# Performance work log

Measured on AMD Instinct MI355X. Metric: run time of the kernel, lower is better.

## Reference

```python
import jax, jax.numpy as jnp
import numpy as np

D_IN = 768
D_MODEL = 768
NUM_HEADS = 12
DEPTH = D_MODEL // NUM_HEADS


def setup_inputs() -> dict:
    key = jax.random.key(0)
    ks = jax.random.split(key, 9)
    B, N = 2, 2048
    s_in = 1.0 / np.sqrt(D_IN)
    s_md = 1.0 / np.sqrt(D_MODEL)
    return {
        "x": jax.random.normal(ks[0], (B, N, D_IN), dtype=jnp.float32),
        "wq": jax.random.normal(ks[1], (D_IN, D_MODEL), dtype=jnp.float32) * s_in,
        "bq": jax.random.normal(ks[2], (D_MODEL,), dtype=jnp.float32) * 0.02,
        "wk": jax.random.normal(ks[3], (D_IN, D_MODEL), dtype=jnp.float32) * s_in,
        "bk": jax.random.normal(ks[4], (D_MODEL,), dtype=jnp.float32) * 0.02,
        "wv": jax.random.normal(ks[5], (D_IN, D_MODEL), dtype=jnp.float32) * s_in,
        "bv": jax.random.normal(ks[6], (D_MODEL,), dtype=jnp.float32) * 0.02,
        "wo": jax.random.normal(ks[7], (D_MODEL, D_MODEL), dtype=jnp.float32) * s_md,
        "bo": jax.random.normal(ks[8], (D_MODEL,), dtype=jnp.float32) * 0.02,
    }


def reference(x, wq, bq, wk, bk, wv, bv, wo, bo):
    B, N, _ = x.shape
    H, D = NUM_HEADS, DEPTH
    # project and split heads: [B,N,H,D] -> [B,H,N,D]
    q = (x @ wq + bq).reshape(B, N, H, D).transpose(0, 2, 1, 3)
    k = (x @ wk + bk).reshape(B, N, H, D).transpose(0, 2, 1, 3)
    v = (x @ wv + bv).reshape(B, N, H, D).transpose(0, 2, 1, 3)
    scale = 1.0 / jnp.sqrt(jnp.asarray(D, dtype=q.dtype))
    attn = jnp.einsum('bhnd,bhmd->bhnm', q, k) * scale  # [B,H,N,N]
    attn = jax.nn.softmax(attn, axis=-1)
    z = jnp.einsum('bhnm,bhmd->bhnd', attn, v)
    z = z.transpose(0, 2, 1, 3).reshape(B, N, H * D)
    return z @ wo + bo
```

## Files before the change

kernel.cpp:

```cpp
#include <hip/hip_runtime.h>
#include <hip/hip_bf16.h>
#include <math.h>

#define NH 12
#define DH 64
#define BB 2
#define NN 2048
#define DM 768

typedef short v8s __attribute__((ext_vector_type(8)));
typedef float v4f __attribute__((ext_vector_type(4)));

__device__ __forceinline__ unsigned short f2bf(float f) {
    union { float f; unsigned u; } x; x.f = f;
    unsigned r = x.u + 0x7fffu + ((x.u >> 16) & 1u);
    return (unsigned short)(r >> 16);
}

__device__ __forceinline__ int cvtpk(float lo, float hi2) {
    int r;
    asm("v_cvt_pk_bf16_f32 %0, %1, %2" : "=v"(r) : "v"(lo), "v"(hi2));
    return r;
}

__device__ __forceinline__ void glds16(const void* g, void* l) {
    __builtin_amdgcn_global_load_lds((const __attribute__((address_space(1))) void*)g,
                                     (__attribute__((address_space(3))) void*)l, 16, 0, 0);
}

__global__ __launch_bounds__(256) void cast_fused_k(
    const float* __restrict__ x, unsigned short* __restrict__ xb,
    const float* __restrict__ w0, const float* __restrict__ w1,
    const float* __restrict__ w2, const float* __restrict__ w3,
    unsigned short* __restrict__ o0, unsigned short* __restrict__ o1,
    unsigned short* __restrict__ o2, unsigned short* __restrict__ o3) {
    __shared__ unsigned short t[64][65];
    int bid = blockIdx.x;
    if (bid < 3072) {
        int i = (bid * 256 + threadIdx.x) * 4;
        float4 v = *(const float4*)(x + i);
        ushort4 o;
        o.x = f2bf(v.x); o.y = f2bf(v.y); o.z = f2bf(v.z); o.w = f2bf(v.w);
        *(ushort4*)(xb + i) = o;
        return;
    }
    int idx = bid - 3072;
    int m = idx / 144, xt = idx % 144;
    const float* in; unsigned short* out;
    switch (m) {
        case 0: in = w0; out = o0; break;
        case 1: in = w1; out = o1; break;
        case 2: in = w2; out = o2; break;
        default: in = w3; out = o3; break;
    }
    int kt = xt / 12, ct = xt % 12;
    int rr = threadIdx.x >> 4, cc = threadIdx.x & 15;
#pragma unroll
    for (int it = 0; it < 4; it++) {
        int row = kt * 64 + it * 16 + rr;
        int col = ct * 64 + cc * 4;
        float4 v = *(const float4*)(in + row * 768 + col);
        t[it * 16 + rr][cc * 4 + 0] = f2bf(v.x);
        t[it * 16 + rr][cc * 4 + 1] = f2bf(v.y);
        t[it * 16 + rr][cc * 4 + 2] = f2bf(v.z);
        t[it * 16 + rr][cc * 4 + 3] = f2bf(v.w);
    }
    __syncthreads();
#pragma unroll
    for (int it = 0; it < 4; it++) {
        int c_l = it * 16 + rr;
        int k_l = cc * 4;
        ushort4 o;
        o.x = t[k_l + 0][c_l];
        o.y = t[k_l + 1][c_l];
        o.z = t[k_l + 2][c_l];
        o.w = t[k_l + 3][c_l];
        *(ushort4*)(out + (ct * 64 + c_l) * 768 + kt * 64 + k_l) = o;
    }
}

__global__ __launch_bounds__(512) void qkv_gemm_k(
    const unsigned short* __restrict__ xb,
    const unsigned short* __restrict__ wqT, const unsigned short* __restrict__ wkT,
    const unsigned short* __restrict__ wvT,
    const float* __restrict__ bq, const float* __restrict__ bk, const float* __restrict__ bv,
    unsigned short* __restrict__ q, unsigned short* __restrict__ k, unsigned short* __restrict__ vT) {
    __shared__ unsigned short Abuf[3][128 * 32];
    __shared__ unsigned short Bbuf[3][128 * 32];

    int lin = blockIdx.x;
    int swz = (lin & 7) * 72 + (lin >> 3);
    int ctile = swz % 18;
    int mtile = swz / 18;
    int mat = ctile / 6;
    int col0 = (ctile % 6) * 128;
    const unsigned short* Bsrc = (mat == 0) ? wqT : ((mat == 1) ? wkT : wvT);
    const float* bias = (mat == 0) ? bq : ((mat == 1) ? bk : bv);

    int tid = threadIdx.x;
    int w = tid >> 6, l = tid & 63;
    int q16 = l & 15, g = l >> 4;
    int wr = w >> 2, wc = w & 3;

    int srow = tid >> 2;
    int ss = tid & 3;
    int c16s = ss ^ ((srow >> 1) & 3);

    auto stage = [&](int tt, int buf) {
        int k0 = tt * 32;
        glds16(xb + (mtile * 128 + srow) * 768 + k0 + (c16s << 3),
               (char*)&Abuf[buf][0] + tid * 16);
        glds16(Bsrc + (col0 + srow) * 768 + k0 + (c16s << 3),
               (char*)&Bbuf[buf][0] + tid * 16);
    };

    v4f zero = {0.f, 0.f, 0.f, 0.f};
    v4f acc[4][2];
#pragma unroll
    for (int i = 0; i < 4; i++)
#pragma unroll
        for (int j = 0; j < 2; j++) acc[i][j] = zero;

    stage(0, 0);
    stage(1, 1);
    asm volatile("s_waitcnt vmcnt(2)" ::: "memory");
    __builtin_amdgcn_s_barrier();
    asm volatile("" ::: "memory");

    int rd = 0;
    for (int tt = 0; tt < 24; ++tt) {
        int st = rd + 2; if (st >= 3) st -= 3;
        if (tt + 2 < 24) stage(tt + 2, st);
        const char* Ab = (const char*)&Abuf[rd][0];
        const char* Bb = (const char*)&Bbuf[rd][0];
        v8s af[4], bf[2];
#pragma unroll
        for (int f = 0; f < 4; f++) {
            int arow = wr * 64 + f * 16 + q16;
            af[f] = *(const v8s*)(Ab + arow * 64 + ((g ^ ((arow >> 1) & 3)) << 4));
        }
#pragma unroll
        for (int j = 0; j < 2; j++) {
            int brow = wc * 32 + j * 16 + q16;
            bf[j] = *(const v8s*)(Bb + brow * 64 + ((g ^ ((brow >> 1) & 3)) << 4));
        }
        __builtin_amdgcn_s_setprio(1);
#pragma unroll
        for (int i = 0; i < 4; i++)
#pragma unroll
            for (int j = 0; j < 2; j++)
                acc[i][j] = __builtin_amdgcn_mfma_f32_16x16x32_bf16(af[i], bf[j], acc[i][j], 0, 0, 0);
        __builtin_amdgcn_s_setprio(0);
        asm volatile("s_waitcnt vmcnt(2)" ::: "memory");
        __builtin_amdgcn_s_barrier();
        asm volatile("" ::: "memory");
        rd = (rd + 1 == 3) ? 0 : rd + 1;
    }

    const float QSCL = 0.125f * 1.44269504088896340736f;
#pragma unroll
    for (int i = 0; i < 4; i++)
#pragma unroll
        for (int j = 0; j < 2; j++)
#pragma unroll
            for (int r = 0; r < 4; r++) {
                int gr = mtile * 128 + wr * 64 + i * 16 + 4 * g + r;
                int gcl = col0 + wc * 32 + j * 16 + q16;
                int b = gr / NN, n = gr % NN;
                int h = gcl / DH, d = gcl % DH;
                int bh = b * NH + h;
                float v = acc[i][j][r] + bias[gcl];
                if (mat == 0)      q[(bh * NN + n) * DH + d]  = f2bf(v * QSCL);
                else if (mat == 1) k[(bh * NN + n) * DH + d]  = f2bf(v);
                else               vT[(bh * DH + d) * NN + n] = f2bf(v);
            }
}

__global__ __launch_bounds__(512) void attn_k(
    const unsigned short* __restrict__ q, const unsigned short* __restrict__ k,
    const unsigned short* __restrict__ vT, unsigned short* __restrict__ z) {
    __shared__ __align__(16) char Kb[2][2][4096];
    __shared__ __align__(16) char Vb[2][2][4096];
    __shared__ unsigned short plds[8][16][36];

    int bh = blockIdx.x % 24;
    int qt = blockIdx.x / 24;
    int b = bh / NH, h = bh % NH;
    int tid = threadIdx.x;
    int w = tid >> 6, l = tid & 63;
    int q16 = l & 15, g = l >> 4;
    int ws = w & 3, hf = w >> 2;

    const unsigned short* qp = q + (size_t)bh * NN * DH;
    const unsigned short* kp = k + (size_t)bh * NN * DH;
    const unsigned short* vp = vT + (size_t)bh * DH * NN;
    int qrow = qt * 64 + ws * 16 + q16;

    v8s qf0 = *(const v8s*)(qp + qrow * DH + 8 * g);
    v8s qf1 = *(const v8s*)(qp + qrow * DH + 32 + 8 * g);

    v8s ones;
#pragma unroll
    for (int i = 0; i < 8; i++) ones[i] = (short)0x3F80;

    int hf_s = tid >> 8;
    int s8 = tid & 255;
    int row_s = s8 >> 3, sl = s8 & 7;
    int kc16 = (sl ^ (row_s & 7)) & 7;
    int vj = sl ^ (row_s & 7);
    int vd = row_s + ((vj >> 2) << 5);
    int vkw = vj & 3;

    auto stage = [&](int t, int buf) {
        int kv0 = hf_s * (NN / 2) + t * 32;
        glds16(kp + (kv0 + row_s) * DH + (kc16 << 3), &Kb[hf_s][buf][s8 * 16]);
        glds16(vp + (size_t)vd * NN + kv0 + vkw * 8, &Vb[hf_s][buf][s8 * 16]);
    };

    v4f zero = {0.f, 0.f, 0.f, 0.f};
    float mrow = -INFINITY;
    v4f o[4];
    v4f osum = zero;
#pragma unroll
    for (int dt = 0; dt < 4; dt++) o[dt] = zero;

    stage(0, 0);
    __syncthreads();

    for (int t = 0; t < 32; ++t) {
        int cur = t & 1;
        if (t + 1 < 32) stage(t + 1, cur ^ 1);

        const char* kb = &Kb[hf][cur][0];
        const char* vb = &Vb[hf][cur][0];

        v4f st[2];
#pragma unroll
        for (int ct = 0; ct < 2; ct++) {
            int krow = ct * 16 + q16;
            v8s kf0 = *(const v8s*)(kb + krow * 128 + ((g ^ (krow & 7)) << 4));
            v8s kf1 = *(const v8s*)(kb + krow * 128 + (((4 + g) ^ (krow & 7)) << 4));
            __builtin_amdgcn_s_setprio(1);
            st[ct] = __builtin_amdgcn_mfma_f32_16x16x32_bf16(kf0, qf0, zero, 0, 0, 0);
            st[ct] = __builtin_amdgcn_mfma_f32_16x16x32_bf16(kf1, qf1, st[ct], 0, 0, 0);
            __builtin_amdgcn_s_setprio(0);
        }

        float ma = fmaxf(fmaxf(st[0][0], st[0][1]), st[0][2]);
        float mb = fmaxf(fmaxf(st[0][3], st[1][0]), st[1][1]);
        float vmax = fmaxf(fmaxf(ma, mb), fmaxf(st[1][2], st[1][3]));
        vmax = fmaxf(vmax, __shfl_xor(vmax, 16));
        vmax = fmaxf(vmax, __shfl_xor(vmax, 32));

        if (!__all(vmax <= mrow + 8.f)) {
            float mn = fmaxf(mrow, vmax);
            float sc = exp2f(mrow - mn);
#pragma unroll
            for (int dt = 0; dt < 4; dt++)
#pragma unroll
                for (int r = 0; r < 4; r++) o[dt][r] *= sc;
            osum[0] *= sc;
            mrow = mn;
        }

#pragma unroll
        for (int ct = 0; ct < 2; ct++) {
            float p0 = exp2f(st[ct][0] - mrow);
            float p1 = exp2f(st[ct][1] - mrow);
            float p2 = exp2f(st[ct][2] - mrow);
            float p3 = exp2f(st[ct][3] - mrow);
            union { int i[2]; short4 s; } u;
            u.i[0] = cvtpk(p0, p1);
            u.i[1] = cvtpk(p2, p3);
            *(short4*)(&plds[w][q16][ct * 16 + 4 * g]) = u.s;
        }

        v8s pf0 = *(const v8s*)(&plds[w][q16][8 * g]);

        osum = __builtin_amdgcn_mfma_f32_16x16x32_bf16(ones, pf0, osum, 0, 0, 0);

        __builtin_amdgcn_s_setprio(1);
#pragma unroll
        for (int dt = 0; dt < 4; dt++) {
            int dcol = dt * 16 + q16;
            int rr = dcol & 31;
            int sl2 = (((dcol >> 5) << 2) + g) ^ (rr & 7);
            v8s vf = *(const v8s*)(vb + rr * 128 + (sl2 << 4));
            o[dt] = __builtin_amdgcn_mfma_f32_16x16x32_bf16(vf, pf0, o[dt], 0, 0, 0);
        }
        __builtin_amdgcn_s_setprio(0);
        __syncthreads();
    }

    float* po = (float*)&Kb[0][0][0];
    float* pm = (float*)&Vb[0][0][0];
    float* pl = pm + 64;
    int row = ws * 16 + q16;

    if (hf == 1) {
#pragma unroll
        for (int dt = 0; dt < 4; dt++)
#pragma unroll
            for (int r = 0; r < 4; r++)
                po[row * 64 + dt * 16 + 4 * g + r] = o[dt][r];
        if (g == 0) { pm[row] = mrow; pl[row] = osum[0]; }
    }
    __syncthreads();
    if (hf == 0) {
        float m1 = pm[row], l1 = pl[row];
        float ms = fmaxf(mrow, m1);
        float a0 = exp2f(mrow - ms), a1 = exp2f(m1 - ms);
        float inv = 1.f / (osum[0] * a0 + l1 * a1);
        int n = qt * 64 + ws * 16 + q16;
#pragma unroll
        for (int dt = 0; dt < 4; dt++) {
            short4 s4;
            s4.x = (short)f2bf((o[dt][0] * a0 + po[row * 64 + dt * 16 + 4 * g + 0] * a1) * inv);
            s4.y = (short)f2bf((o[dt][1] * a0 + po[row * 64 + dt * 16 + 4 * g + 1] * a1) * inv);
            s4.z = (short)f2bf((o[dt][2] * a0 + po[row * 64 + dt * 16 + 4 * g + 2] * a1) * inv);
            s4.w = (short)f2bf((o[dt][3] * a0 + po[row * 64 + dt * 16 + 4 * g + 3] * a1) * inv);
            *(short4*)(&z[((size_t)(b * NN + n)) * DM + h * DH + dt * 16 + 4 * g]) = s4;
        }
    }
}

__global__ __launch_bounds__(512) void out_gemm_k(
    const unsigned short* __restrict__ zb, const unsigned short* __restrict__ woT,
    const float* __restrict__ bo, float* __restrict__ out) {
    __shared__ unsigned short Abuf[3][128 * 32];
    __shared__ unsigned short Bbuf[3][128 * 32];

    int lin = blockIdx.x;
    int swz = (lin & 7) * 24 + (lin >> 3);
    int ctile = swz % 6;
    int mtile = swz / 6;
    int col0 = ctile * 128;

    int tid = threadIdx.x;
    int w = tid >> 6, l = tid & 63;
    int q16 = l & 15, g = l >> 4;
    int wr = w >> 2, wc = w & 3;

    int srow = tid >> 2;
    int ss = tid & 3;
    int c16s = ss ^ ((srow >> 1) & 3);

    auto stage = [&](int tt, int buf) {
        int k0 = tt * 32;
        glds16(zb + (mtile * 128 + srow) * 768 + k0 + (c16s << 3),
               (char*)&Abuf[buf][0] + tid * 16);
        glds16(woT + (col0 + srow) * 768 + k0 + (c16s << 3),
               (char*)&Bbuf[buf][0] + tid * 16);
    };

    v4f zero = {0.f, 0.f, 0.f, 0.f};
    v4f acc[4][2];
#pragma unroll
    for (int i = 0; i < 4; i++)
#pragma unroll
        for (int j = 0; j < 2; j++) acc[i][j] = zero;

    stage(0, 0);
    stage(1, 1);
    asm volatile("s_waitcnt vmcnt(2)" ::: "memory");
    __builtin_amdgcn_s_barrier();
    asm volatile("" ::: "memory");

    int rd = 0;
    for (int tt = 0; tt < 24; ++tt) {
        int st = rd + 2; if (st >= 3) st -= 3;
        if (tt + 2 < 24) stage(tt + 2, st);
        const char* Ab = (const char*)&Abuf[rd][0];
        const char* Bb = (const char*)&Bbuf[rd][0];
        v8s af[4], bf[2];
#pragma unroll
        for (int f = 0; f < 4; f++) {
            int arow = wr * 64 + f * 16 + q16;
            af[f] = *(const v8s*)(Ab + arow * 64 + ((g ^ ((arow >> 1) & 3)) << 4));
        }
#pragma unroll
        for (int j = 0; j < 2; j++) {
            int brow = wc * 32 + j * 16 + q16;
            bf[j] = *(const v8s*)(Bb + brow * 64 + ((g ^ ((brow >> 1) & 3)) << 4));
        }
        __builtin_amdgcn_s_setprio(1);
#pragma unroll
        for (int i = 0; i < 4; i++)
#pragma unroll
            for (int j = 0; j < 2; j++)
                acc[i][j] = __builtin_amdgcn_mfma_f32_16x16x32_bf16(af[i], bf[j], acc[i][j], 0, 0, 0);
        __builtin_amdgcn_s_setprio(0);
        asm volatile("s_waitcnt vmcnt(2)" ::: "memory");
        __builtin_amdgcn_s_barrier();
        asm volatile("" ::: "memory");
        rd = (rd + 1 == 3) ? 0 : rd + 1;
    }

#pragma unroll
    for (int i = 0; i < 4; i++)
#pragma unroll
        for (int j = 0; j < 2; j++)
#pragma unroll
            for (int r = 0; r < 4; r++) {
                int gr = mtile * 128 + wr * 64 + i * 16 + 4 * g + r;
                int gc = col0 + wc * 32 + j * 16 + q16;
                out[gr * 768 + gc] = acc[i][j][r] + bo[gc];
            }
}

extern "C" void kernel_launch(void* const* d_in, const int* in_sizes, int n_in,
                              void* d_out, int out_size, void* d_ws, size_t ws_size,
                              hipStream_t stream) {
    const float* x  = (const float*)d_in[0];
    const float* wq = (const float*)d_in[1];
    const float* bq = (const float*)d_in[2];
    const float* wk = (const float*)d_in[3];
    const float* bk = (const float*)d_in[4];
    const float* wv = (const float*)d_in[5];
    const float* bv = (const float*)d_in[6];
    const float* wo = (const float*)d_in[7];
    const float* bo = (const float*)d_in[8];
    float* out = (float*)d_out;

    const int NX = BB * NN * DM;
    const int NW = 768 * 768;

    unsigned short* wsp = (unsigned short*)d_ws;
    unsigned short* xb  = wsp;
    unsigned short* wqT = xb + NX;
    unsigned short* wkT = wqT + NW;
    unsigned short* wvT = wkT + NW;
    unsigned short* woT = wvT + NW;
    unsigned short* qb  = woT + NW;
    unsigned short* kb  = qb + NX;
    unsigned short* vTb = kb + NX;
    unsigned short* zb  = vTb + NX;

    cast_fused_k<<<3648, 256, 0, stream>>>(x, xb, wq, wk, wv, wo, wqT, wkT, wvT, woT);
    qkv_gemm_k<<<576, 512, 0, stream>>>(xb, wqT, wkT, wvT, bq, bk, bv, qb, kb, vTb);
    attn_k<<<BB * NH * (NN / 64), 512, 0, stream>>>(qb, kb, vTb, zb);
    out_gemm_k<<<192, 512, 0, stream>>>(zb, woT, bo, out);
}
```

Baseline: 116.6 us.

## Rewrite attention kernel with 32x32x16 MFMA and four-way KV split

The attention kernel moves from 16x16x32 MFMA tiles to 32x32x16 tiles. Each wave now owns 32 query rows, and the KV sequence is split four ways instead of two, with a four-way merge of partial softmax states through shared memory at the end. P fragments are built in registers with cross-lane shuffles instead of a round trip through LDS, and the row sum is computed with VALU adds instead of a ones-matrix MFMA. The aim is fewer instructions and LDS traffic per FLOP. In exchange it uses 64KB of shared memory and relies on more complex bpermute-based rescaling and epilogue logic.

```diff
diff --git a/kernel.cpp b/kernel.cpp
--- a/kernel.cpp
+++ b/kernel.cpp
@@ -10,6 +10,7 @@
 
 typedef short v8s __attribute__((ext_vector_type(8)));
 typedef float v4f __attribute__((ext_vector_type(4)));
+typedef float v16f __attribute__((ext_vector_type(16)));
 
 __device__ __forceinline__ unsigned short f2bf(float f) {
     union { float f; unsigned u; } x; x.f = f;
@@ -176,150 +177,182 @@
             }
 }
 
+#define MKFRAG(PC, BASE, FR) {                                                     \
+    int a0 = cvtpk(PC[BASE + 0], PC[BASE + 1]), a1 = cvtpk(PC[BASE + 2], PC[BASE + 3]); \
+    int b0 = cvtpk(PC[BASE + 4], PC[BASE + 5]), b1 = cvtpk(PC[BASE + 6], PC[BASE + 7]); \
+    int t0 = hi ? a0 : b0, t1 = hi ? a1 : b1;                                      \
+    int r0 = __shfl_xor(t0, 32), r1 = __shfl_xor(t1, 32);                          \
+    union { int i[4]; v8s s; } u_;                                                 \
+    u_.i[0] = hi ? r0 : a0; u_.i[1] = hi ? r1 : a1;                                \
+    u_.i[2] = hi ? b0 : r0; u_.i[3] = hi ? b1 : r1;                                \
+    FR = u_.s; }
+
 __global__ __launch_bounds__(512) void attn_k(
     const unsigned short* __restrict__ q, const unsigned short* __restrict__ k,
     const unsigned short* __restrict__ vT, unsigned short* __restrict__ z) {
-    __shared__ __align__(16) char Kb[2][2][4096];
-    __shared__ __align__(16) char Vb[2][2][4096];
-    __shared__ unsigned short plds[8][16][36];
+    __shared__ __align__(16) char smem[65536];
 
     int bh = blockIdx.x % 24;
     int qt = blockIdx.x / 24;
     int b = bh / NH, h = bh % NH;
     int tid = threadIdx.x;
     int w = tid >> 6, l = tid & 63;
-    int q16 = l & 15, g = l >> 4;
-    int ws = w & 3, hf = w >> 2;
+    int ln = l & 31, hi = l >> 5;
+    int qd = w & 3, strip = w >> 2;
 
     const unsigned short* qp = q + (size_t)bh * NN * DH;
     const unsigned short* kp = k + (size_t)bh * NN * DH;
     const unsigned short* vp = vT + (size_t)bh * DH * NN;
-    int qrow = qt * 64 + ws * 16 + q16;
-
-    v8s qf0 = *(const v8s*)(qp + qrow * DH + 8 * g);
-    v8s qf1 = *(const v8s*)(qp + qrow * DH + 32 + 8 * g);
-
-    v8s ones;
-#pragma unroll
-    for (int i = 0; i < 8; i++) ones[i] = (short)0x3F80;
-
-    int hf_s = tid >> 8;
-    int s8 = tid & 255;
-    int row_s = s8 >> 3, sl = s8 & 7;
-    int kc16 = (sl ^ (row_s & 7)) & 7;
-    int vj = sl ^ (row_s & 7);
-    int vd = row_s + ((vj >> 2) << 5);
-    int vkw = vj & 3;
-
+
+    int qrow = qt * 64 + strip * 32 + ln;
+    v8s qf[4];
+#pragma unroll
+    for (int ks = 0; ks < 4; ++ks)
+        qf[ks] = *(const v8s*)(qp + qrow * DH + 16 * ks + 8 * hi);
+
+    int sq = tid >> 7;
+    int s7 = tid & 127;
     auto stage = [&](int t, int buf) {
-        int kv0 = hf_s * (NN / 2) + t * 32;
-        glds16(kp + (kv0 + row_s) * DH + (kc16 << 3), &Kb[hf_s][buf][s8 * 16]);
-        glds16(vp + (size_t)vd * NN + kv0 + vkw * 8, &Vb[hf_s][buf][s8 * 16]);
+        int kv0 = sq * (NN / 4) + t * 32;
+#pragma unroll
+        for (int i = 0; i < 2; ++i) {
+            int slot = s7 + 128 * i;
+            int row = slot >> 3, psl = slot & 7;
+            int j = psl ^ (row & 7);
+            glds16(kp + (kv0 + row) * DH + (j << 3),
+                   smem + sq * 8192 + buf * 4096 + slot * 16);
+            int vd = row + ((j >> 2) << 5);
+            glds16(vp + (size_t)vd * NN + kv0 + ((j & 3) << 3),
+                   smem + 32768 + sq * 8192 + buf * 4096 + slot * 16);
+        }
     };
 
-    v4f zero = {0.f, 0.f, 0.f, 0.f};
-    float mrow = -INFINITY;
-    v4f o[4];
-    v4f osum = zero;
-#pragma unroll
-    for (int dt = 0; dt < 4; dt++) o[dt] = zero;
+    v16f o0, o1;
+#pragma unroll
+    for (int i = 0; i < 16; i++) { o0[i] = 0.f; o1[i] = 0.f; }
+    float mrow = -INFINITY, lsum = 0.f;
 
     stage(0, 0);
     __syncthreads();
 
-    for (int t = 0; t < 32; ++t) {
+    for (int t = 0; t < 16; ++t) {
         int cur = t & 1;
-        if (t + 1 < 32) stage(t + 1, cur ^ 1);
-
-        const char* kb = &Kb[hf][cur][0];
-        const char* vb = &Vb[hf][cur][0];
-
-        v4f st[2];
-#pragma unroll
-        for (int ct = 0; ct < 2; ct++) {
-            int krow = ct * 16 + q16;
-            v8s kf0 = *(const v8s*)(kb + krow * 128 + ((g ^ (krow & 7)) << 4));
-            v8s kf1 = *(const v8s*)(kb + krow * 128 + (((4 + g) ^ (krow & 7)) << 4));
+        if (t + 1 < 16) stage(t + 1, cur ^ 1);
+        const char* kb = smem + qd * 8192 + cur * 4096;
+        const char* vb = smem + 32768 + qd * 8192 + cur * 4096;
+
+        v16f s;
+#pragma unroll
+        for (int i = 0; i < 16; i++) s[i] = 0.f;
+        {
+            v8s kf[4];
+#pragma unroll
+            for (int ks = 0; ks < 4; ++ks)
+                kf[ks] = *(const v8s*)(kb + ln * 128 + (((2 * ks + hi) ^ (ln & 7)) << 4));
             __builtin_amdgcn_s_setprio(1);
-            st[ct] = __builtin_amdgcn_mfma_f32_16x16x32_bf16(kf0, qf0, zero, 0, 0, 0);
-            st[ct] = __builtin_amdgcn_mfma_f32_16x16x32_bf16(kf1, qf1, st[ct], 0, 0, 0);
+#pragma unroll
+            for (int ks = 0; ks < 4; ++ks)
+                s = __builtin_amdgcn_mfma_f32_32x32x16_bf16(kf[ks], qf[ks], s, 0, 0, 0);
             __builtin_amdgcn_s_setprio(0);
         }
 
-        float ma = fmaxf(fmaxf(st[0][0], st[0][1]), st[0][2]);
-        float mb = fmaxf(fmaxf(st[0][3], st[1][0]), st[1][1]);
-        float vmax = fmaxf(fmaxf(ma, mb), fmaxf(st[1][2], st[1][3]));
-        vmax = fmaxf(vmax, __shfl_xor(vmax, 16));
+        float x0 = -1e30f, x1 = -1e30f, x2 = -1e30f, x3 = -1e30f;
+#pragma unroll
+        for (int i = 0; i < 16; i += 4) {
+            x0 = fmaxf(x0, s[i]);     x1 = fmaxf(x1, s[i + 1]);
+            x2 = fmaxf(x2, s[i + 2]); x3 = fmaxf(x3, s[i + 3]);
+        }
+        float vmax = fmaxf(fmaxf(x0, x1), fmaxf(x2, x3));
         vmax = fmaxf(vmax, __shfl_xor(vmax, 32));
 
         if (!__all(vmax <= mrow + 8.f)) {
             float mn = fmaxf(mrow, vmax);
             float sc = exp2f(mrow - mn);
 #pragma unroll
-            for (int dt = 0; dt < 4; dt++)
-#pragma unroll
-                for (int r = 0; r < 4; r++) o[dt][r] *= sc;
-            osum[0] *= sc;
+            for (int r = 0; r < 16; ++r) {
+                int addr = 4 * ((r & 3) + 8 * (r >> 2)) + (hi << 4);
+                float scr = __uint_as_float(
+                    __builtin_amdgcn_ds_bpermute(addr, __float_as_uint(sc)));
+                o0[r] *= scr; o1[r] *= scr;
+            }
+            lsum *= sc;
             mrow = mn;
         }
 
-#pragma unroll
-        for (int ct = 0; ct < 2; ct++) {
-            float p0 = exp2f(st[ct][0] - mrow);
-            float p1 = exp2f(st[ct][1] - mrow);
-            float p2 = exp2f(st[ct][2] - mrow);
-            float p3 = exp2f(st[ct][3] - mrow);
-            union { int i[2]; short4 s; } u;
-            u.i[0] = cvtpk(p0, p1);
-            u.i[1] = cvtpk(p2, p3);
-            *(short4*)(&plds[w][q16][ct * 16 + 4 * g]) = u.s;
-        }
-
-        v8s pf0 = *(const v8s*)(&plds[w][q16][8 * g]);
-
-        osum = __builtin_amdgcn_mfma_f32_16x16x32_bf16(ones, pf0, osum, 0, 0, 0);
-
-        __builtin_amdgcn_s_setprio(1);
-#pragma unroll
-        for (int dt = 0; dt < 4; dt++) {
-            int dcol = dt * 16 + q16;
-            int rr = dcol & 31;
-            int sl2 = (((dcol >> 5) << 2) + g) ^ (rr & 7);
-            v8s vf = *(const v8s*)(vb + rr * 128 + (sl2 << 4));
-            o[dt] = __builtin_amdgcn_mfma_f32_16x16x32_bf16(vf, pf0, o[dt], 0, 0, 0);
-        }
-        __builtin_amdgcn_s_setprio(0);
+        float r0 = 0.f, r1 = 0.f, r2 = 0.f, r3 = 0.f;
+#pragma unroll
+        for (int i = 0; i < 16; i += 4) {
+            s[i] = exp2f(s[i] - mrow);         s[i + 1] = exp2f(s[i + 1] - mrow);
+            s[i + 2] = exp2f(s[i + 2] - mrow); s[i + 3] = exp2f(s[i + 3] - mrow);
+            r0 += s[i]; r1 += s[i + 1]; r2 += s[i + 2]; r3 += s[i + 3];
+        }
+        float rs = (r0 + r1) + (r2 + r3);
+        rs += __shfl_xor(rs, 32);
+        lsum += rs;
+
+        v8s pf[2];
+        MKFRAG(s, 0, pf[0]);
+        MKFRAG(s, 8, pf[1]);
+
+        {
+            v8s vf0[2], vf1[2];
+#pragma unroll
+            for (int ks = 0; ks < 2; ++ks) {
+                vf0[ks] = *(const v8s*)(vb + ln * 128 + (((2 * ks + hi) ^ (ln & 7)) << 4));
+                vf1[ks] = *(const v8s*)(vb + ln * 128 + (((4 + 2 * ks + hi) ^ (ln & 7)) << 4));
+            }
+            __builtin_amdgcn_s_setprio(1);
+#pragma unroll
+            for (int ks = 0; ks < 2; ++ks) {
+                o0 = __builtin_amdgcn_mfma_f32_32x32x16_bf16(pf[ks], vf0[ks], o0, 0, 0, 0);
+                o1 = __builtin_amdgcn_mfma_f32_32x32x16_bf16(pf[ks], vf1[ks], o1, 0, 0, 0);
+            }
+            __builtin_amdgcn_s_setprio(0);
+        }
         __syncthreads();
     }
 
-    float* po = (float*)&Kb[0][0][0];
-    float* pm = (float*)&Vb[0][0][0];
-    float* pl = pm + 64;
-    int row = ws * 16 + q16;
-
-    if (hf == 1) {
-#pragma unroll
-        for (int dt = 0; dt < 4; dt++)
-#pragma unroll
-            for (int r = 0; r < 4; r++)
-                po[row * 64 + dt * 16 + 4 * g + r] = o[dt][r];
-        if (g == 0) { pm[row] = mrow; pl[row] = osum[0]; }
+    float* po = (float*)smem;
+    float* pml = (float*)(smem + 49152);
+    int qg = strip * 32 + ln;
+
+    if (qd != 0) {
+#pragma unroll
+        for (int r = 0; r < 16; ++r) {
+            int qr = (r & 3) + 8 * (r >> 2) + 4 * hi;
+            int row = strip * 32 + qr;
+            po[((qd - 1) * 64 + row) * 64 + ln]      = o0[r];
+            po[((qd - 1) * 64 + row) * 64 + 32 + ln] = o1[r];
+        }
+        pml[(0 * 4 + qd) * 64 + qg] = mrow;
+        pml[(1 * 4 + qd) * 64 + qg] = lsum;
     }
     __syncthreads();
-    if (hf == 0) {
-        float m1 = pm[row], l1 = pl[row];
-        float ms = fmaxf(mrow, m1);
-        float a0 = exp2f(mrow - ms), a1 = exp2f(m1 - ms);
-        float inv = 1.f / (osum[0] * a0 + l1 * a1);
-        int n = qt * 64 + ws * 16 + q16;
-#pragma unroll
-        for (int dt = 0; dt < 4; dt++) {
-            short4 s4;
-            s4.x = (short)f2bf((o[dt][0] * a0 + po[row * 64 + dt * 16 + 4 * g + 0] * a1) * inv);
-            s4.y = (short)f2bf((o[dt][1] * a0 + po[row * 64 + dt * 16 + 4 * g + 1] * a1) * inv);
-            s4.z = (short)f2bf((o[dt][2] * a0 + po[row * 64 + dt * 16 + 4 * g + 2] * a1) * inv);
-            s4.w = (short)f2bf((o[dt][3] * a0 + po[row * 64 + dt * 16 + 4 * g + 3] * a1) * inv);
-            *(short4*)(&z[((size_t)(b * NN + n)) * DM + h * DH + dt * 16 + 4 * g]) = s4;
+    if (qd == 0) {
+        float m1 = pml[(0 * 4 + 1) * 64 + qg], l1 = pml[(1 * 4 + 1) * 64 + qg];
+        float m2 = pml[(0 * 4 + 2) * 64 + qg], l2 = pml[(1 * 4 + 2) * 64 + qg];
+        float m3 = pml[(0 * 4 + 3) * 64 + qg], l3 = pml[(1 * 4 + 3) * 64 + qg];
+        float M = fmaxf(fmaxf(mrow, m1), fmaxf(m2, m3));
+        float w0 = exp2f(mrow - M), w1_ = exp2f(m1 - M);
+        float w2_ = exp2f(m2 - M), w3_ = exp2f(m3 - M);
+        float inv = 1.f / (lsum * w0 + l1 * w1_ + l2 * w2_ + l3 * w3_);
+        w0 *= inv; w1_ *= inv; w2_ *= inv; w3_ *= inv;
+#pragma unroll
+        for (int r = 0; r < 16; ++r) {
+            int qr = (r & 3) + 8 * (r >> 2) + 4 * hi;
+            int addr = qr * 4;
+            float W0 = __uint_as_float(__builtin_amdgcn_ds_bpermute(addr, __float_as_uint(w0)));
+            float W1 = __uint_as_float(__builtin_amdgcn_ds_bpermute(addr, __float_as_uint(w1_)));
+            float W2 = __uint_as_float(__builtin_amdgcn_ds_bpermute(addr, __float_as_uint(w2_)));
+            float W3 = __uint_as_float(__builtin_amdgcn_ds_bpermute(addr, __float_as_uint(w3_)));
+            int row = strip * 32 + qr;
+            float z0 = o0[r] * W0 + po[(0 * 64 + row) * 64 + ln] * W1
+                     + po[(1 * 64 + row) * 64 + ln] * W2 + po[(2 * 64 + row) * 64 + ln] * W3;
+            float z1 = o1[r] * W0 + po[(0 * 64 + row) * 64 + 32 + ln] * W1
+                     + po[(1 * 64 + row) * 64 + 32 + ln] * W2 + po[(2 * 64 + row) * 64 + 32 + ln] * W3;
+            int n = qt * 64 + row;
+            z[((size_t)(b * NN + n)) * DM + h * DH + ln]      = f2bf(z0);
+            z[((size_t)(b * NN + n)) * DM + h * DH + 32 + ln] = f2bf(z1);
         }
     }
 }
```

Result: slower. 119.2 us (+2.2%).
